# Kernel tuning notes

Hardware: AMD Instinct MI355X
Metric: run time of the kernel (lower is better)

Reference implementation:

```python
import jax, jax.numpy as jnp
import numpy as np

B, S, D_MODEL, H = 2, 2048, 1024, 16
HD = D_MODEL // H  # 64
EPS = 1e-6


def setup_inputs() -> dict:
    key = jax.random.key(0)
    ks = jax.random.split(key, 8)
    x = jax.random.normal(ks[0], (B, S, D_MODEL), dtype=jnp.float32)
    # Proper RoPE rotation angles: theta_i = pos / 10000^(2i/head_dim)
    inv_freq = 1.0 / (10000.0 ** (np.arange(0, HD, 2, dtype=np.float32) / HD))  # (HD/2,)
    angles = np.arange(S, dtype=np.float32)[:, None] * inv_freq[None, :]        # (S, HD/2)
    rope_cos = jnp.asarray(np.cos(angles))
    rope_sin = jnp.asarray(np.sin(angles))
    w_std = 1.0 / np.sqrt(D_MODEL)
    wq = jax.random.normal(ks[1], (D_MODEL, D_MODEL), dtype=jnp.float32) * w_std
    wk = jax.random.normal(ks[2], (D_MODEL, D_MODEL), dtype=jnp.float32) * w_std
    wv = jax.random.normal(ks[3], (D_MODEL, D_MODEL), dtype=jnp.float32) * w_std
    wo = jax.random.normal(ks[4], (D_MODEL, D_MODEL), dtype=jnp.float32) * w_std
    q_scale = 1.0 + 0.02 * jax.random.normal(ks[5], (HD,), dtype=jnp.float32)
    k_scale = 1.0 + 0.02 * jax.random.normal(ks[6], (HD,), dtype=jnp.float32)
    return {"x": x, "wq": wq, "wk": wk, "wv": wv, "wo": wo,
            "q_scale": q_scale, "k_scale": k_scale,
            "rope_cos": rope_cos, "rope_sin": rope_sin}


def _rmsnorm(t, scale):
    # RMSNorm over head_dim
    var = jnp.mean(jnp.square(t), axis=-1, keepdims=True)
    return t * jax.lax.rsqrt(var + EPS) * scale


def _apply_rope(t, cos, sin):
    # t: (B,S,H,HD); interpret consecutive pairs as complex (real, imag)
    b, s, h, d = t.shape
    tp = t.reshape(b, s, h, d // 2, 2)
    tr, ti = tp[..., 0], tp[..., 1]
    c = cos[None, :, None, :]  # (1,S,1,HD/2)
    sn = sin[None, :, None, :]
    or_ = tr * c - ti * sn
    oi = tr * sn + ti * c
    return jnp.stack([or_, oi], axis=-1).reshape(b, s, h, d)


def reference(x, wq, wk, wv, wo, q_scale, k_scale, rope_cos, rope_sin):
    b, s, _ = x.shape
    # Torch-style linear: y = x @ W^T, W is (out, in)
    q = jnp.einsum('bsd,od->bso', x, wq).reshape(b, s, H, HD)
    k = jnp.einsum('bsd,od->bso', x, wk).reshape(b, s, H, HD)
    v = jnp.einsum('bsd,od->bso', x, wv).reshape(b, s, H, HD)
    q = _apply_rope(_rmsnorm(q, q_scale), rope_cos, rope_sin)
    k = _apply_rope(_rmsnorm(k, k_scale), rope_cos, rope_sin)
    # scaled dot-product attention (no mask), fp32 softmax
    scale = 1.0 / np.sqrt(HD)
    scores = jnp.einsum('bqhd,bkhd->bhqk', q, k) * scale
    probs = jax.nn.softmax(scores.astype(jnp.float32), axis=-1)
    attn = jnp.einsum('bhqk,bkhd->bqhd', probs, v).reshape(b, s, D_MODEL)
    return jnp.einsum('bso,do->bsd', attn, wo.T).astype(x.dtype) if False else jnp.einsum('bsd,od->bso', attn, wo)
```

## Files before the change

kernel.cpp:

```cpp
#include <hip/hip_runtime.h>
#include <hip/hip_bf16.h>


#define B_ 2
#define S_ 2048
#define D_ 1024
#define H_ 16
#define HD_ 64
#define M_ (B_*S_)

typedef __attribute__((ext_vector_type(8))) short short8;
typedef __attribute__((ext_vector_type(4))) short short4v;
typedef __attribute__((ext_vector_type(4))) float f32x4;
typedef __attribute__((ext_vector_type(4))) _Float16 half4;
typedef __attribute__((ext_vector_type(8))) _Float16 half8;

static __device__ __forceinline__ short f2bf(float f) {
    __hip_bfloat16 h = __float2bfloat16(f);
    return *reinterpret_cast<short*>(&h);
}
static __device__ __forceinline__ short f2h(float f) {
    _Float16 h = (_Float16)f;
    return *reinterpret_cast<short*>(&h);
}
static __device__ __forceinline__ float bf2f(short s) {
    unsigned u = ((unsigned)(unsigned short)s) << 16;
    float f; __builtin_memcpy(&f, &u, 4); return f;
}

typedef __attribute__((address_space(1))) const unsigned int gu32_t;
typedef __attribute__((address_space(3))) unsigned int lu32_t;
static __device__ __forceinline__ void gld16(const short* g, short* l) {
    __builtin_amdgcn_global_load_lds((gu32_t*)g, (lu32_t*)l, 16, 0, 0);
}

__global__ __launch_bounds__(256)
void convert_bf16(const float* __restrict__ x,
                  const float* __restrict__ wq, const float* __restrict__ wk,
                  const float* __restrict__ wv, const float* __restrict__ wo,
                  short* __restrict__ xb, short* __restrict__ wqkvb, short* __restrict__ wob)
{
    const size_t t4 = ((size_t)blockIdx.x * 256 + threadIdx.x) * 4;
    const float* src; short* dst; size_t off, doff;
    if (t4 < 4194304)      { src = x;  dst = xb;    off = t4;           doff = t4; }
    else if (t4 < 5242880) { src = wq; dst = wqkvb; off = t4 - 4194304; doff = t4 - 4194304; }
    else if (t4 < 6291456) { src = wk; dst = wqkvb; off = t4 - 5242880; doff = t4 - 4194304; }
    else if (t4 < 7340032) { src = wv; dst = wqkvb; off = t4 - 6291456; doff = t4 - 4194304; }
    else                   { src = wo; dst = wob;   off = t4 - 7340032; doff = t4 - 7340032; }
    float4 v = *(const float4*)(src + off);
    short4v s = { f2bf(v.x), f2bf(v.y), f2bf(v.z), f2bf(v.w) };
    *(short4v*)(dst + doff) = s;
}

__global__ __launch_bounds__(256)
void gemm_qkv(const short* __restrict__ A, const short* __restrict__ Bw,
              short* __restrict__ Qb, short* __restrict__ Kb, short* __restrict__ Vt)
{
    __shared__ __align__(16) short As[128*32];
    __shared__ __align__(16) short Bs[128*32];
    const int tid = threadIdx.x;
    const int w = tid >> 6, lane = tid & 63, quad = lane >> 4, l16 = lane & 15;
    const int wr = w >> 1, wc = w & 1;
    const int bm0 = blockIdx.x * 128, bn0 = blockIdx.y * 128;

    const int srow = tid >> 2;
    const int skch = (tid & 3) * 8;
    const short* gA0 = A  + (size_t)(bm0 + srow) * 1024 + skch;
    const short* gA1 = A  + (size_t)(bm0 + 64 + srow) * 1024 + skch;
    const short* gB0 = Bw + (size_t)(bn0 + srow) * 1024 + skch;
    const short* gB1 = Bw + (size_t)(bn0 + 64 + srow) * 1024 + skch;
    short* lA0 = As + w*512;
    short* lA1 = As + 2048 + w*512;
    short* lB0 = Bs + w*512;
    short* lB1 = Bs + 2048 + w*512;

    f32x4 acc[4][4];
    #pragma unroll
    for (int i = 0; i < 4; ++i)
        #pragma unroll
        for (int j = 0; j < 4; ++j) acc[i][j] = (f32x4){0.f,0.f,0.f,0.f};

    for (int k0 = 0; k0 < 1024; k0 += 32) {
        __syncthreads();
        gld16(gA0 + k0, lA0);
        gld16(gA1 + k0, lA1);
        gld16(gB0 + k0, lB0);
        gld16(gB1 + k0, lB1);
        __syncthreads();
        short8 af[4], bfr[4];
        #pragma unroll
        for (int i = 0; i < 4; ++i)
            af[i] = *(const short8*)(As + (wr*64 + i*16 + l16)*32 + quad*8);
        #pragma unroll
        for (int j = 0; j < 4; ++j)
            bfr[j] = *(const short8*)(Bs + (wc*64 + j*16 + l16)*32 + quad*8);
        #pragma unroll
        for (int i = 0; i < 4; ++i)
            #pragma unroll
            for (int j = 0; j < 4; ++j)
                acc[i][j] = __builtin_amdgcn_mfma_f32_16x16x32_bf16(af[i], bfr[j], acc[i][j], 0, 0, 0);
    }

    #pragma unroll
    for (int i = 0; i < 4; ++i) {
        #pragma unroll
        for (int r = 0; r < 4; ++r) {
            const int m = bm0 + wr*64 + i*16 + quad*4 + r;
            #pragma unroll
            for (int j = 0; j < 4; ++j) {
                const int n = bn0 + wc*64 + j*16 + l16;
                const float v = acc[i][j][r];
                const int which = n >> 10, nn = n & 1023;
                const int h = nn >> 6, hd = nn & 63;
                const int b = m >> 11, s = m & (S_-1);
                if (which == 0)      Qb[(((size_t)b*H_ + h)*S_ + s)*HD_ + hd] = f2bf(v);
                else if (which == 1) Kb[(((size_t)b*H_ + h)*S_ + s)*HD_ + hd] = f2bf(v);
                else                 Vt[(((size_t)b*H_ + h)*HD_ + hd)*S_ + s] = f2h(v);
            }
        }
    }
}

__global__ __launch_bounds__(256)
void gemm_out(const short* __restrict__ po, const float* __restrict__ pl,
              const short* __restrict__ Bw, float* __restrict__ C)
{
    __shared__ __align__(16) short As[64*32];
    __shared__ __align__(16) short Bs[128*32];
    const int tid = threadIdx.x;
    const int w = tid >> 6, lane = tid & 63, quad = lane >> 4, l16 = lane & 15;
    const int bm0 = blockIdx.x * 64, bn0 = blockIdx.y * 128;

    const int srow = tid >> 2;
    const int skch = (tid & 3) * 8;
    const int m = bm0 + srow;
    const int b = m >> 11, s = m & (S_-1);
    const short* gB0 = Bw + (size_t)(bn0 + srow) * 1024 + skch;
    const short* gB1 = Bw + (size_t)(bn0 + 64 + srow) * 1024 + skch;
    short* lB0 = Bs + w*512;
    short* lB1 = Bs + 2048 + w*512;

    float inv[16];
    #pragma unroll
    for (int h = 0; h < 16; ++h)
        inv[h] = 1.0f / (pl[((size_t)(b*16 + h))*S_ + s] + pl[65536 + ((size_t)(b*16 + h))*S_ + s]);

    f32x4 acc[4][2];
    #pragma unroll
    for (int i = 0; i < 4; ++i) {
        acc[i][0] = (f32x4){0.f,0.f,0.f,0.f};
        acc[i][1] = (f32x4){0.f,0.f,0.f,0.f};
    }

    for (int k0 = 0; k0 < 1024; k0 += 32) {
        const int h = k0 >> 6;
        half8 p0 = *(const half8*)(po +            (size_t)m*1024 + k0 + skch);
        half8 p1 = *(const half8*)(po + 4194304 + (size_t)m*1024 + k0 + skch);
        short8 a;
        #pragma unroll
        for (int j = 0; j < 8; ++j)
            a[j] = f2bf(((float)p0[j] + (float)p1[j]) * inv[h]);
        __syncthreads();
        *(short8*)(As + srow*32 + skch) = a;
        gld16(gB0 + k0, lB0);
        gld16(gB1 + k0, lB1);
        __syncthreads();
        short8 af[4], bfr[2];
        #pragma unroll
        for (int i = 0; i < 4; ++i)
            af[i] = *(const short8*)(As + (i*16 + l16)*32 + quad*8);
        #pragma unroll
        for (int j = 0; j < 2; ++j)
            bfr[j] = *(const short8*)(Bs + (w*32 + j*16 + l16)*32 + quad*8);
        #pragma unroll
        for (int i = 0; i < 4; ++i)
            #pragma unroll
            for (int j = 0; j < 2; ++j)
                acc[i][j] = __builtin_amdgcn_mfma_f32_16x16x32_bf16(af[i], bfr[j], acc[i][j], 0, 0, 0);
    }

    #pragma unroll
    for (int i = 0; i < 4; ++i)
        #pragma unroll
        for (int r = 0; r < 4; ++r) {
            const int mm = bm0 + i*16 + quad*4 + r;
            #pragma unroll
            for (int j = 0; j < 2; ++j) {
                const int n = bn0 + w*32 + j*16 + l16;
                C[(size_t)mm*1024 + n] = acc[i][j][r];
            }
        }
}

__global__ __launch_bounds__(256)
void rmsnorm_rope(short* __restrict__ qbh, short* __restrict__ kbh,
                  const float* __restrict__ q_scale, const float* __restrict__ k_scale,
                  const float* __restrict__ rope_cos, const float* __restrict__ rope_sin)
{
    const int lane = threadIdx.x & 63;
    const int wid  = threadIdx.x >> 6;
    const int row  = blockIdx.x * 4 + wid;
    const bool isq = (blockIdx.y == 0);
    short* t = isq ? qbh : kbh;
    const float* sc = isq ? q_scale : k_scale;
    const int s = row & (S_-1);
    float v = bf2f(t[(size_t)row * HD_ + lane]);
    float ssum = v * v;
    #pragma unroll
    for (int m = 32; m >= 1; m >>= 1) ssum += __shfl_xor(ssum, m, 64);
    float r = rsqrtf(ssum * (1.0f/64.0f) + 1e-6f);
    float nv = v * r * sc[lane];
    const int p = lane >> 1;
    float c  = rope_cos[s*32 + p];
    float sn = rope_sin[s*32 + p];
    float partner = __shfl_xor(nv, 1, 64);
    float outv = (lane & 1) ? (partner * sn + nv * c) : (nv * c - partner * sn);
    if (isq) outv *= 0.18033688011112042f;
    t[(size_t)row * HD_ + lane] = f2bf(outv);
}

__global__ __launch_bounds__(256, 2)
void flash_mfma(const short* __restrict__ qb, const short* __restrict__ kb,
                const short* __restrict__ vt, short* __restrict__ po, float* __restrict__ pl)
{
    __shared__ __align__(16) short Ks[64*64];
    __shared__ __align__(16) short Vs[64*64];

    const int tid  = threadIdx.x;
    const int wv   = tid >> 6;
    const int lane = tid & 63;
    const int quad = lane >> 4;
    const int l16  = lane & 15;
    const int bh   = blockIdx.y;
    const int b    = bh >> 4, h = bh & (H_-1);
    const int q0   = blockIdx.x * 128 + wv * 32;
    const int sp   = blockIdx.z;
    const int kt0  = sp * 1024;
    const size_t hbase = (size_t)bh * S_ * HD_;
    const size_t vbase = (size_t)bh * HD_ * S_;
    short* po_sp = po + (size_t)sp * 4194304;
    float* pl_sp = pl + (size_t)sp * 65536;

    const int c0r = tid >> 3,       c0c = tid & 7;
    const int c1r = (tid+256) >> 3, c1c = (tid+256) & 7;

    short8 qfrag[2][2];
    #pragma unroll
    for (int qf = 0; qf < 2; ++qf)
        #pragma unroll
        for (int c = 0; c < 2; ++c)
            qfrag[qf][c] = *(const short8*)(qb + hbase + (size_t)(q0 + qf*16 + l16)*HD_ + c*32 + quad*8);

    f32x4 Oacc[2][4];
    #pragma unroll
    for (int qf = 0; qf < 2; ++qf)
        #pragma unroll
        for (int dt = 0; dt < 4; ++dt) Oacc[qf][dt] = (f32x4){0.f,0.f,0.f,0.f};
    float l_lane[2] = {0.f, 0.f};

    short8 rk0 = *(const short8*)(kb + hbase + (size_t)(kt0 + c0r)*HD_ + c0c*8);
    short8 rk1 = *(const short8*)(kb + hbase + (size_t)(kt0 + c1r)*HD_ + c1c*8);
    short8 rv0 = *(const short8*)(vt + vbase + (size_t)c0r*S_ + kt0 + c0c*8);
    short8 rv1 = *(const short8*)(vt + vbase + (size_t)c1r*S_ + kt0 + c1c*8);

    #pragma unroll 1
    for (int t = 0; t < 16; ++t) {
        __syncthreads();
        *(short8*)(Ks + c0r*64 + ((c0c ^ (c0r & 7)) << 3)) = rk0;
        *(short8*)(Ks + c1r*64 + ((c1c ^ (c1r & 7)) << 3)) = rk1;
        *(short8*)(Vs + c0r*64 + ((c0c ^ (c0r & 7)) << 3)) = rv0;
        *(short8*)(Vs + c1r*64 + ((c1c ^ (c1r & 7)) << 3)) = rv1;
        __syncthreads();
        if (t < 15) {
            const int ktn = kt0 + (t+1)*64;
            rk0 = *(const short8*)(kb + hbase + (size_t)(ktn + c0r)*HD_ + c0c*8);
            rk1 = *(const short8*)(kb + hbase + (size_t)(ktn + c1r)*HD_ + c1c*8);
            rv0 = *(const short8*)(vt + vbase + (size_t)c0r*S_ + ktn + c0c*8);
            rv1 = *(const short8*)(vt + vbase + (size_t)c1r*S_ + ktn + c1c*8);
        }

        #pragma unroll
        for (int st = 0; st < 4; ++st) {
            short8 kf0 = *(const short8*)(Ks + (st*16 + l16)*64 + (((quad    ) ^ (l16 & 7)) << 3));
            short8 kf1 = *(const short8*)(Ks + (st*16 + l16)*64 + (((4 + quad) ^ (l16 & 7)) << 3));
            const int ch16 = st*2 + (quad >> 1);
            const int sw   = ((ch16 ^ (l16 & 7)) << 3) + (quad & 1)*4;
            half4 va[4];
            #pragma unroll
            for (int dt = 0; dt < 4; ++dt)
                va[dt] = *(const half4*)(Vs + (dt*16 + l16)*64 + sw);
            #pragma unroll
            for (int qf = 0; qf < 2; ++qf) {
                f32x4 acc = (f32x4){0.f,0.f,0.f,0.f};
                acc = __builtin_amdgcn_mfma_f32_16x16x32_bf16(kf0, qfrag[qf][0], acc, 0, 0, 0);
                acc = __builtin_amdgcn_mfma_f32_16x16x32_bf16(kf1, qfrag[qf][1], acc, 0, 0, 0);
                half4 pb;
                #pragma unroll
                for (int r = 0; r < 4; ++r) {
                    float p = __builtin_amdgcn_exp2f(acc[r] - 12.0f);
                    l_lane[qf] += p;
                    pb[r] = (_Float16)p;
                }
                #pragma unroll
                for (int dt = 0; dt < 4; ++dt)
                    Oacc[qf][dt] = __builtin_amdgcn_mfma_f32_16x16x16f16(va[dt], pb, Oacc[qf][dt], 0, 0, 0);
            }
        }
    }

    #pragma unroll
    for (int qf = 0; qf < 2; ++qf) {
        l_lane[qf] += __shfl_xor(l_lane[qf], 16, 64);
        l_lane[qf] += __shfl_xor(l_lane[qf], 32, 64);
        if (quad == 0) pl_sp[(size_t)bh*S_ + q0 + qf*16 + l16] = l_lane[qf];
    }
    #pragma unroll
    for (int qf = 0; qf < 2; ++qf) {
        const int s = q0 + qf*16 + l16;
        #pragma unroll
        for (int dt = 0; dt < 4; ++dt) {
            short4v o;
            #pragma unroll
            for (int r = 0; r < 4; ++r) o[r] = f2h(Oacc[qf][dt][r]);
            *(short4v*)(po_sp + (((size_t)b*S_ + s)*H_ + h)*HD_ + dt*16 + quad*4) = o;
        }
    }
}

extern "C" void kernel_launch(void* const* d_in, const int* in_sizes, int n_in,
                              void* d_out, int out_size, void* d_ws, size_t ws_size,
                              hipStream_t stream)
{
    (void)in_sizes; (void)n_in; (void)out_size; (void)ws_size;
    const float* x        = (const float*)d_in[0];
    const float* wq       = (const float*)d_in[1];
    const float* wk       = (const float*)d_in[2];
    const float* wv       = (const float*)d_in[3];
    const float* wo       = (const float*)d_in[4];
    const float* q_scale  = (const float*)d_in[5];
    const float* k_scale  = (const float*)d_in[6];
    const float* rope_cos = (const float*)d_in[7];
    const float* rope_sin = (const float*)d_in[8];
    float* out = (float*)d_out;
    short* ws  = (short*)d_ws;

    short* qbh   = ws;
    short* kbh   = ws + 4194304;
    short* vt    = ws + 8388608;
    short* xb    = ws + 16777216;
    short* wqkvb = ws + 20971520;
    short* wob   = ws + 24117248;
    short* po    = ws + 25165824;
    float* pl    = (float*)(ws + 33554432);

    convert_bf16<<<dim3(8192), 256, 0, stream>>>(x, wq, wk, wv, wo, xb, wqkvb, wob);
    gemm_qkv<<<dim3(M_/128, 24), 256, 0, stream>>>(xb, wqkvb, qbh, kbh, vt);
    rmsnorm_rope<<<dim3(B_*H_*S_/4, 2), 256, 0, stream>>>(qbh, kbh, q_scale, k_scale, rope_cos, rope_sin);
    flash_mfma<<<dim3(S_/128, B_*H_, 2), 256, 0, stream>>>(qbh, kbh, vt, po, pl);
    gemm_out<<<dim3(M_/64, D_/128), 256, 0, stream>>>(po, pl, wob, out);
}
```

Measured before the change: 222.6 us.

## Split flash attention KV into four chunks with XCD-aware block mapping

```diff
diff --git a/kernel.cpp b/kernel.cpp
--- a/kernel.cpp
+++ b/kernel.cpp
@@ -8,6 +8,8 @@
 #define H_ 16
 #define HD_ 64
 #define M_ (B_*S_)
+#define SPLIT_ 4
+#define KSPAN_ (S_/SPLIT_)
 
 typedef __attribute__((ext_vector_type(8))) short short8;
 typedef __attribute__((ext_vector_type(4))) short short4v;
@@ -142,8 +144,13 @@
 
     float inv[16];
     #pragma unroll
-    for (int h = 0; h < 16; ++h)
-        inv[h] = 1.0f / (pl[((size_t)(b*16 + h))*S_ + s] + pl[65536 + ((size_t)(b*16 + h))*S_ + s]);
+    for (int h = 0; h < 16; ++h) {
+        float l = 0.f;
+        #pragma unroll
+        for (int sp = 0; sp < SPLIT_; ++sp)
+            l += pl[(size_t)sp*65536 + ((size_t)(b*16 + h))*S_ + s];
+        inv[h] = 1.0f / l;
+    }
 
     f32x4 acc[4][2];
     #pragma unroll
@@ -154,12 +161,14 @@
 
     for (int k0 = 0; k0 < 1024; k0 += 32) {
         const int h = k0 >> 6;
-        half8 p0 = *(const half8*)(po +            (size_t)m*1024 + k0 + skch);
-        half8 p1 = *(const half8*)(po + 4194304 + (size_t)m*1024 + k0 + skch);
+        half8 p0 = *(const half8*)(po + 0ull*4194304 + (size_t)m*1024 + k0 + skch);
+        half8 p1 = *(const half8*)(po + 1ull*4194304 + (size_t)m*1024 + k0 + skch);
+        half8 p2 = *(const half8*)(po + 2ull*4194304 + (size_t)m*1024 + k0 + skch);
+        half8 p3 = *(const half8*)(po + 3ull*4194304 + (size_t)m*1024 + k0 + skch);
         short8 a;
         #pragma unroll
         for (int j = 0; j < 8; ++j)
-            a[j] = f2bf(((float)p0[j] + (float)p1[j]) * inv[h]);
+            a[j] = f2bf((((float)p0[j] + (float)p1[j]) + ((float)p2[j] + (float)p3[j])) * inv[h]);
         __syncthreads();
         *(short8*)(As + srow*32 + skch) = a;
         gld16(gB0 + k0, lB0);
@@ -219,23 +228,29 @@
     t[(size_t)row * HD_ + lane] = f2bf(outv);
 }
 
-__global__ __launch_bounds__(256, 2)
+__global__ __launch_bounds__(256)
 void flash_mfma(const short* __restrict__ qb, const short* __restrict__ kb,
                 const short* __restrict__ vt, short* __restrict__ po, float* __restrict__ pl)
 {
     __shared__ __align__(16) short Ks[64*64];
     __shared__ __align__(16) short Vs[64*64];
+
+    const int id   = blockIdx.x;
+    const int xcd  = id & 7;
+    const int rest = id >> 3;
+    const int qblk = rest & 15;
+    const int g    = (rest >> 4) * 8 + xcd;
+    const int bh   = g >> 2;
+    const int sp   = g & 3;
 
     const int tid  = threadIdx.x;
     const int wv   = tid >> 6;
     const int lane = tid & 63;
     const int quad = lane >> 4;
     const int l16  = lane & 15;
-    const int bh   = blockIdx.y;
     const int b    = bh >> 4, h = bh & (H_-1);
-    const int q0   = blockIdx.x * 128 + wv * 32;
-    const int sp   = blockIdx.z;
-    const int kt0  = sp * 1024;
+    const int q0   = qblk * 128 + wv * 32;
+    const int kt0  = sp * KSPAN_;
     const size_t hbase = (size_t)bh * S_ * HD_;
     const size_t vbase = (size_t)bh * HD_ * S_;
     short* po_sp = po + (size_t)sp * 4194304;
@@ -264,14 +279,14 @@
     short8 rv1 = *(const short8*)(vt + vbase + (size_t)c1r*S_ + kt0 + c1c*8);
 
     #pragma unroll 1
-    for (int t = 0; t < 16; ++t) {
+    for (int t = 0; t < KSPAN_/64; ++t) {
         __syncthreads();
         *(short8*)(Ks + c0r*64 + ((c0c ^ (c0r & 7)) << 3)) = rk0;
         *(short8*)(Ks + c1r*64 + ((c1c ^ (c1r & 7)) << 3)) = rk1;
         *(short8*)(Vs + c0r*64 + ((c0c ^ (c0r & 7)) << 3)) = rv0;
         *(short8*)(Vs + c1r*64 + ((c1c ^ (c1r & 7)) << 3)) = rv1;
         __syncthreads();
-        if (t < 15) {
+        if (t < KSPAN_/64 - 1) {
             const int ktn = kt0 + (t+1)*64;
             rk0 = *(const short8*)(kb + hbase + (size_t)(ktn + c0r)*HD_ + c0c*8);
             rk1 = *(const short8*)(kb + hbase + (size_t)(ktn + c1r)*HD_ + c1c*8);
@@ -351,11 +366,11 @@
     short* wqkvb = ws + 20971520;
     short* wob   = ws + 24117248;
     short* po    = ws + 25165824;
-    float* pl    = (float*)(ws + 33554432);
+    float* pl    = (float*)(ws + 41943040);
 
     convert_bf16<<<dim3(8192), 256, 0, stream>>>(x, wq, wk, wv, wo, xb, wqkvb, wob);
     gemm_qkv<<<dim3(M_/128, 24), 256, 0, stream>>>(xb, wqkvb, qbh, kbh, vt);
     rmsnorm_rope<<<dim3(B_*H_*S_/4, 2), 256, 0, stream>>>(qbh, kbh, q_scale, k_scale, rope_cos, rope_sin);
-    flash_mfma<<<dim3(S_/128, B_*H_, 2), 256, 0, stream>>>(qbh, kbh, vt, po, pl);
+    flash_mfma<<<dim3((S_/128)*B_*H_*SPLIT_), 256, 0, stream>>>(qbh, kbh, vt, po, pl);
     gemm_out<<<dim3(M_/64, D_/128), 256, 0, stream>>>(po, pl, wob, out);
 }
```

Measured after the change: 231.5 us. 4.0% more time.
